# Kernel optimization log

Hardware: AMD Instinct MI355X
Metric: run time of the kernel (lower is better)

The kernel has to match this reference:

```python
import jax, jax.numpy as jnp
import numpy as np

HEADS = 4
DIM_QK = 128
DIM_V = 128
FMAP = 32  # H = W = 32, L = 1024
DIM = 512
B = 16


def rel_to_abs(x):
    # x: [B, Nh, L, 2L-1] -> [B, Nh, L, L]
    b, nh, L, _ = x.shape
    x = jnp.pad(x, ((0, 0), (0, 0), (0, 0), (0, 1)))          # [B, Nh, L, 2L]
    flat = x.reshape(b, nh, L * 2 * L)
    flat = jnp.pad(flat, ((0, 0), (0, 0), (0, L - 1)))
    final = flat.reshape(b, nh, L + 1, 2 * L - 1)
    return final[:, :, :L, L - 1:]


def relative_logits_1d(q, rel_k):
    # q: [B, Nh, H, W, d], rel_k: [2W-1, d] -> [B, Nh, H, H, W, W]
    b, nh, h, w, _ = q.shape
    rl = jnp.einsum('bnhwd,md->bnhwm', q, rel_k)
    rl = rl.reshape(b, nh * h, w, 2 * w - 1)
    rl = rel_to_abs(rl)                                        # [B, Nh*H, W, W]
    rl = rl.reshape(b, nh, h, w, w)
    rl = jnp.broadcast_to(rl[:, :, :, None], (b, nh, h, h, w, w))
    return rl


def rel_pos_logits(q, rel_height, rel_width):
    # q: [B, Nh, L, d] with L = FMAP*FMAP -> [B, Nh, L, L]
    b, nh, L, d = q.shape
    h = w = FMAP
    q5 = q.reshape(b, nh, h, w, d)
    # width logits: 'b n x i y j -> b n (x y) (i j)'
    rw = relative_logits_1d(q5, rel_width)
    rw = rw.transpose(0, 1, 2, 4, 3, 5).reshape(b, nh, h * w, h * w)
    # height logits: transpose spatial, then 'b n x i y j -> b n (y x) (j i)'
    rh = relative_logits_1d(q5.transpose(0, 1, 3, 2, 4), rel_height)
    rh = rh.transpose(0, 1, 4, 2, 5, 3).reshape(b, nh, h * w, h * w)
    return rw + rh


def setup_inputs() -> dict:
    key = jax.random.key(0)
    k1, k2, k3, k4, k5 = jax.random.split(key, 5)
    scale = DIM_QK ** -0.5
    return {
        'featuremap': jax.random.normal(k1, (B, DIM, FMAP, FMAP), jnp.float32),
        'w_qk': jax.random.normal(k2, (2 * HEADS * DIM_QK, DIM), jnp.float32) * (DIM ** -0.5),
        'w_v': jax.random.normal(k3, (HEADS * DIM_V, DIM), jnp.float32) * (DIM ** -0.5),
        'rel_height': jax.random.normal(k4, (2 * FMAP - 1, DIM_QK), jnp.float32) * scale,
        'rel_width': jax.random.normal(k5, (2 * FMAP - 1, DIM_QK), jnp.float32) * scale,
    }


def reference(featuremap, w_qk, w_v, rel_height, rel_width):
    b, c, h, w = featuremap.shape
    L = h * w
    # 1x1 convs (no bias) == channel matmuls
    qk = jnp.einsum('bchw,oc->bohw', featuremap, w_qk)
    q, k = jnp.split(qk, 2, axis=1)
    v = jnp.einsum('bchw,oc->bohw', featuremap, w_v)

    def to_heads(x, d):
        # 'B (h d) H W -> B h (H W) d'
        return x.reshape(b, HEADS, d, L).transpose(0, 1, 3, 2)

    q = to_heads(q, DIM_QK) * (DIM_QK ** -0.5)
    k = to_heads(k, DIM_QK)
    v = to_heads(v, DIM_V)

    logits = jnp.einsum('bhxd,bhyd->bhxy', q, k)
    logits = logits + rel_pos_logits(q, rel_height, rel_width)
    weights = jax.nn.softmax(logits, axis=-1)
    attn = jnp.einsum('bhxy,bhyd->bhxd', weights, v)
    # 'B h (H W) d -> B (h d) H W'
    out = attn.transpose(0, 1, 3, 2).reshape(b, HEADS * DIM_V, h, w)
    return out
```

## Files before the change

### kernel.cpp

```cpp
#include <hip/hip_runtime.h>
#include <hip/hip_bf16.h>
#include <math.h>

typedef __bf16 bf16x8 __attribute__((ext_vector_type(8)));
typedef float f32x4 __attribute__((ext_vector_type(4)));

#define QSCALE_L2E (0.08838834764831845f * 1.4426950408889634f)

static __device__ __forceinline__ unsigned short bits_bf16(float v) {
  __hip_bfloat16 h = __float2bfloat16(v);
  return *reinterpret_cast<unsigned short*>(&h);
}

static __device__ __forceinline__ void gload16(const void* g, void* l) {
  __builtin_amdgcn_global_load_lds(
      (const __attribute__((address_space(1))) void*)g,
      (__attribute__((address_space(3))) void*)l, 16, 0, 0);
}

__global__ __launch_bounds__(256) void k_convw(const float* __restrict__ wqk,
                                               const float* __restrict__ wv,
                                               const float* __restrict__ relw,
                                               const float* __restrict__ relh,
                                               __hip_bfloat16* __restrict__ wall,
                                               __hip_bfloat16* __restrict__ relsb) {
  int i = blockIdx.x * 256 + threadIdx.x;
  if (i < 1536 * 512) {
    float v = (i < 1024 * 512) ? wqk[i] : wv[i - 1024 * 512];
    wall[i] = __float2bfloat16(v);
  } else {
    int j = i - 1536 * 512;
    int t = j >> 13, m = (j >> 7) & 63, d = j & 127;
    float v = (m < 63) ? (t ? relh[m * 128 + d] : relw[m * 128 + d]) : 0.f;
    relsb[j] = __float2bfloat16(v);
  }
}

__global__ __launch_bounds__(256) void k_tfm(const float* __restrict__ fm,
                                             __hip_bfloat16* __restrict__ fmt) {
  __shared__ float t[64][65];
  int lt = blockIdx.x, ct = blockIdx.y, b = blockIdx.z;
  int tid = threadIdx.x;
  const float* src = fm + ((size_t)b * 512 + ct * 64) * 1024 + lt * 64;
#pragma unroll
  for (int i = 0; i < 16; ++i) {
    int idx = i * 256 + tid;
    int r = idx >> 6, cl = idx & 63;
    t[r][cl] = src[(size_t)r * 1024 + cl];
  }
  __syncthreads();
  __hip_bfloat16* dst = fmt + ((size_t)b * 1024 + lt * 64) * 512 + ct * 64;
#pragma unroll
  for (int i = 0; i < 16; ++i) {
    int idx = i * 256 + tid;
    int r = idx >> 6, cc = idx & 63;
    dst[(size_t)r * 512 + cc] = __float2bfloat16(t[cc][r]);
  }
}

__global__ __launch_bounds__(256) void k_gemm(const __hip_bfloat16* __restrict__ fmt,
                                              const __hip_bfloat16* __restrict__ wall,
                                              __hip_bfloat16* __restrict__ Qb,
                                              __hip_bfloat16* __restrict__ Kb,
                                              __hip_bfloat16* __restrict__ Vt) {
  __shared__ char smem[32768];
  char* As = smem;
  char* Bs = smem + 16384;
  int bm = blockIdx.x, bn = blockIdx.y, b = blockIdx.z;
  int tid = threadIdx.x;
  int lane = tid & 63, wave = tid >> 6;
  int wr = wave >> 1, wc = wave & 1;
  int g = lane >> 4, ln = lane & 15;
  const char* Ag = (const char*)(fmt + ((size_t)b * 1024 + bm * 128) * 512);
  const char* Bg = (const char*)(wall + (size_t)bn * 128 * 512);

  int j3 = lane >> 3, j7 = lane & 7;
  int segsrc = ((j7 ^ j3) << 4);

  f32x4 acc[4][4] = {};
  for (int kb = 0; kb < 8; ++kb) {
#pragma unroll
    for (int i = 0; i < 4; ++i) {
      int R = (wave * 4 + i) * 8;
      size_t go = (size_t)(R + j3) * 1024 + (size_t)kb * 128 + segsrc;
      gload16(Ag + go, As + R * 128);
      gload16(Bg + go, Bs + R * 128);
    }
    __syncthreads();
#pragma unroll
    for (int ks = 0; ks < 2; ++ks) {
      int kcol = ks * 64 + (g << 4);
      bf16x8 af[4], bfr[4];
#pragma unroll
      for (int m = 0; m < 4; ++m) {
        int row = wr * 64 + m * 16 + ln;
        af[m] = *(const bf16x8*)(As + row * 128 + (kcol ^ ((ln & 7) << 4)));
      }
#pragma unroll
      for (int n = 0; n < 4; ++n) {
        int row = wc * 64 + n * 16 + ln;
        bfr[n] = *(const bf16x8*)(Bs + row * 128 + (kcol ^ ((ln & 7) << 4)));
      }
#pragma unroll
      for (int m = 0; m < 4; ++m)
#pragma unroll
        for (int n = 0; n < 4; ++n)
          acc[m][n] = __builtin_amdgcn_mfma_f32_16x16x32_bf16(af[m], bfr[n], acc[m][n], 0, 0, 0);
    }
    __syncthreads();
  }

  int otype = bn >> 2;
  int head = bn & 3;
  if (otype != 2) {
    float sc = (otype == 0) ? QSCALE_L2E : 1.0f;
#pragma unroll
    for (int m = 0; m < 4; ++m)
#pragma unroll
      for (int n = 0; n < 4; ++n) {
        int d = wc * 64 + n * 16 + ln;
#pragma unroll
        for (int r = 0; r < 4; ++r) {
          int l = wr * 64 + m * 16 + g * 4 + r;
          *(__hip_bfloat16*)(smem + l * 256 + ((d * 2) ^ ((l & 7) << 4))) =
              __float2bfloat16(acc[m][n][r] * sc);
        }
      }
    __syncthreads();
    __hip_bfloat16* dstb =
        (otype == 0 ? Qb : Kb) + (((size_t)(b * 4 + head) * 1024) + bm * 128) * 128;
#pragma unroll
    for (int i = 0; i < 8; ++i) {
      int idx = i * 256 + tid;
      int row = idx >> 4, c16 = idx & 15;
      uint4 v = *(const uint4*)(smem + row * 256 + ((c16 * 16) ^ ((row & 7) << 4)));
      *(uint4*)(dstb + (size_t)row * 128 + c16 * 8) = v;
    }
  } else {
#pragma unroll
    for (int m = 0; m < 4; ++m)
#pragma unroll
      for (int n = 0; n < 4; ++n) {
        int d = wc * 64 + n * 16 + ln;
        int lbase = wr * 64 + m * 16 + g * 4;
        ushort4 pk;
        pk.x = bits_bf16(acc[m][n][0]);
        pk.y = bits_bf16(acc[m][n][1]);
        pk.z = bits_bf16(acc[m][n][2]);
        pk.w = bits_bf16(acc[m][n][3]);
        *(ushort4*)(smem + d * 256 + ((lbase * 2) ^ ((d & 7) << 4))) = pk;
      }
    __syncthreads();
    __hip_bfloat16* dstb = Vt + ((size_t)(b * 4 + head) * 128) * 1024 + bm * 128;
#pragma unroll
    for (int i = 0; i < 8; ++i) {
      int idx = i * 256 + tid;
      int row = idx >> 4, c16 = idx & 15;
      uint4 v = *(const uint4*)(smem + row * 256 + ((c16 * 16) ^ ((row & 7) << 4)));
      *(uint4*)(dstb + (size_t)row * 1024 + c16 * 8) = v;
    }
  }
}

__global__ __launch_bounds__(256) void k_bias(const __hip_bfloat16* __restrict__ Qb,
                                              const __hip_bfloat16* __restrict__ relsb,
                                              float* __restrict__ QRW,
                                              float* __restrict__ QRH) {
  __shared__ char sh[32768];
  int bx = blockIdx.x, bh = blockIdx.y;
  int tid = threadIdx.x, lane = tid & 63, wave = tid >> 6;
  int g = lane >> 4, ln = lane & 15;
#pragma unroll
  for (int i = 0; i < 8; ++i) {
    int chunk = i * 256 + tid;
    int row = chunk >> 4, c16 = chunk & 15;
    *(uint4*)(sh + row * 256 + ((c16 * 16) ^ ((row & 7) << 4))) =
        *(const uint4*)(relsb + (size_t)row * 128 + c16 * 8);
  }
  __syncthreads();
  size_t bhL = (size_t)bh * 1024;
  int l0 = bx * 128 + wave * 32;
  const __hip_bfloat16* Qg = Qb + (bhL + l0) * 128;
  bf16x8 a[2][4];
#pragma unroll
  for (int lf = 0; lf < 2; ++lf)
#pragma unroll
    for (int ks = 0; ks < 4; ++ks)
      a[lf][ks] = *(const bf16x8*)(Qg + (size_t)(lf * 16 + ln) * 128 + ks * 32 + g * 8);
#pragma unroll
  for (int t = 0; t < 2; ++t) {
    float* dst = (t == 0 ? QRW : QRH) + (bhL + l0) * 64;
#pragma unroll
    for (int n = 0; n < 4; ++n) {
      f32x4 acc2[2] = {};
#pragma unroll
      for (int ks = 0; ks < 4; ++ks) {
        int mrow = n * 16 + ln;
        bf16x8 bf = *(const bf16x8*)(sh + t * 16384 + mrow * 256 +
                                     ((ks * 64 + g * 16) ^ ((mrow & 7) << 4)));
#pragma unroll
        for (int lf = 0; lf < 2; ++lf)
          acc2[lf] = __builtin_amdgcn_mfma_f32_16x16x32_bf16(a[lf][ks], bf, acc2[lf], 0, 0, 0);
      }
#pragma unroll
      for (int lf = 0; lf < 2; ++lf)
#pragma unroll
        for (int r = 0; r < 4; ++r)
          dst[(size_t)(lf * 16 + g * 4 + r) * 64 + n * 16 + ln] = acc2[lf][r];
    }
  }
}

__global__ __launch_bounds__(512, 2) void k_attn(const __hip_bfloat16* __restrict__ Qb,
                                                 const __hip_bfloat16* __restrict__ Kb,
                                                 const __hip_bfloat16* __restrict__ Vt,
                                                 const float* __restrict__ QRW,
                                                 const float* __restrict__ QRH,
                                                 float* __restrict__ out) {
  extern __shared__ char smem[];
  float* hb_s = (float*)smem;
  char* kbuf = smem + 40960;
  char* vbuf = smem + 40960 + 32768;
  char* pt = smem + 40960 + 65536;

  int bh = blockIdx.x, qt = blockIdx.y;
  int b = bh >> 2, h = bh & 3;
  int tid = threadIdx.x, lane = tid & 63, wave = tid >> 6;
  int g = lane >> 4, ln = lane & 15;
  int q0 = qt * 256;
  size_t bhL = (size_t)bh * 1024;

#pragma unroll
  for (int i = 0; i < 5; ++i) {
    int c = i * 512 + tid;
    if (c < 2304) {
      int row = c / 9, j = c % 9;
      int s0 = (31 - ((q0 + row) >> 5)) & ~3;
      *(uint4*)(hb_s + row * 40 + j * 4) =
          *(const uint4*)(QRH + (bhL + q0 + row) * 64 + s0 + j * 4);
    }
  }

  bf16x8 qa[2][4];
  float wb[2][2][4];
  int qloc[2], hbase[2];
#pragma unroll
  for (int u = 0; u < 2; ++u) {
    qloc[u] = wave * 32 + u * 16 + ln;
    int qg = q0 + qloc[u];
    int cx = qg & 31, rx = qg >> 5;
    hbase[u] = (31 - rx) & 3;
    const __hip_bfloat16* qrow = Qb + (bhL + qg) * 128;
#pragma unroll
    for (int ks = 0; ks < 4; ++ks)
      qa[u][ks] = *(const bf16x8*)(qrow + ks * 32 + g * 8);
    const float* wrow = QRW + (bhL + qg) * 64 + (31 - cx) + g * 4;
#pragma unroll
    for (int half = 0; half < 2; ++half)
#pragma unroll
      for (int r = 0; r < 4; ++r) wb[u][half][r] = wrow[half * 16 + r];
  }

  const char* Kg0 = (const char*)(Kb + bhL * 128);
  const char* Vg0 = (const char*)(Vt + (size_t)bh * 128 * 1024);
  int j3 = lane >> 3, j7 = lane & 7;
  int segv = ((j7 ^ j3) << 4);

  auto STAGE = [&](int bsel, int kt2) {
    const char* Kg = Kg0 + (size_t)kt2 * 64 * 256;
    char* kvb = kbuf + bsel * 16384;
#pragma unroll
    for (int i = 0; i < 2; ++i) {
      int R = (wave * 2 + i) * 4;
      int seg = ((lane & 15) ^ ((i & 1) * 4 + (lane >> 4))) << 4;
      gload16(Kg + (size_t)(R + (lane >> 4)) * 256 + seg, kvb + R * 256);
    }
    const char* Vg = Vg0 + (size_t)kt2 * 128;
    char* vtb = vbuf + bsel * 16384;
#pragma unroll
    for (int i = 0; i < 2; ++i) {
      int R = (wave * 2 + i) * 8;
      gload16(Vg + (size_t)(R + j3) * 2048 + segv, vtb + R * 128);
    }
  };

  f32x4 acc[2][8] = {};
  float mrow[2] = {-1e30f, -1e30f}, lrow[2] = {0.f, 0.f};
  char* pw = pt + wave * 4096;

  STAGE(0, 0);
  __syncthreads();

  for (int kt = 0; kt < 16; ++kt) {
    int cur = kt & 1;
    if (kt < 15) STAGE(cur ^ 1, kt + 1);
    char* kvb = kbuf + cur * 16384;
    char* vtb = vbuf + cur * 16384;

    f32x4 s[2][4] = {};
    __builtin_amdgcn_s_setprio(1);
#pragma unroll
    for (int ks = 0; ks < 4; ++ks) {
      int kcol = ks * 64 + (g << 4);
#pragma unroll
      for (int n = 0; n < 4; ++n) {
        int krow = n * 16 + ln;
        bf16x8 kf = *(const bf16x8*)(kvb + krow * 256 + (kcol ^ ((krow & 7) << 4)));
        s[0][n] = __builtin_amdgcn_mfma_f32_16x16x32_bf16(kf, qa[0][ks], s[0][n], 0, 0, 0);
        s[1][n] = __builtin_amdgcn_mfma_f32_16x16x32_bf16(kf, qa[1][ks], s[1][n], 0, 0, 0);
      }
    }
    __builtin_amdgcn_s_setprio(0);
#pragma unroll
    for (int u = 0; u < 2; ++u) {
      float hb0 = hb_s[qloc[u] * 40 + hbase[u] + kt * 2];
      float hb1 = hb_s[qloc[u] * 40 + hbase[u] + kt * 2 + 1];
#pragma unroll
      for (int n = 0; n < 4; ++n) {
        float hb = (n >> 1) ? hb1 : hb0;
#pragma unroll
        for (int r = 0; r < 4; ++r) s[u][n][r] += wb[u][n & 1][r] + hb;
      }
      float mt = s[u][0][0];
#pragma unroll
      for (int n = 0; n < 4; ++n)
#pragma unroll
        for (int r = 0; r < 4; ++r) mt = fmaxf(mt, s[u][n][r]);
      mt = fmaxf(mt, __shfl_xor(mt, 16, 64));
      mt = fmaxf(mt, __shfl_xor(mt, 32, 64));
      float mn = fmaxf(mrow[u], mt);
      float alpha = exp2f(mrow[u] - mn);
      mrow[u] = mn;
      float rs = 0.f;
#pragma unroll
      for (int n = 0; n < 4; ++n)
#pragma unroll
        for (int r = 0; r < 4; ++r) {
          s[u][n][r] = exp2f(s[u][n][r] - mn);
          rs += s[u][n][r];
        }
      rs += __shfl_xor(rs, 16, 64);
      rs += __shfl_xor(rs, 32, 64);
      lrow[u] = lrow[u] * alpha + rs;
#pragma unroll
      for (int mf = 0; mf < 8; ++mf) acc[u][mf] *= alpha;
#pragma unroll
      for (int n = 0; n < 4; ++n) {
        ushort4 pk;
        pk.x = bits_bf16(s[u][n][0]);
        pk.y = bits_bf16(s[u][n][1]);
        pk.z = bits_bf16(s[u][n][2]);
        pk.w = bits_bf16(s[u][n][3]);
        *(ushort4*)(pw + (u * 16 + ln) * 128 + ((n * 32 + g * 8) ^ ((ln & 7) << 4))) = pk;
      }
    }
    __builtin_amdgcn_s_setprio(1);
#pragma unroll
    for (int ks2 = 0; ks2 < 2; ++ks2) {
      int kcb = ks2 * 64 + (g << 4);
      bf16x8 pb0 = *(const bf16x8*)(pw + ln * 128 + (kcb ^ ((ln & 7) << 4)));
      bf16x8 pb1 = *(const bf16x8*)(pw + (16 + ln) * 128 + (kcb ^ ((ln & 7) << 4)));
#pragma unroll
      for (int mf = 0; mf < 8; ++mf) {
        int vrow = mf * 16 + ln;
        bf16x8 av = *(const bf16x8*)(vtb + vrow * 128 + (kcb ^ ((vrow & 7) << 4)));
        acc[0][mf] = __builtin_amdgcn_mfma_f32_16x16x32_bf16(av, pb0, acc[0][mf], 0, 0, 0);
        acc[1][mf] = __builtin_amdgcn_mfma_f32_16x16x32_bf16(av, pb1, acc[1][mf], 0, 0, 0);
      }
    }
    __builtin_amdgcn_s_setprio(0);
    __syncthreads();
  }
#pragma unroll
  for (int u = 0; u < 2; ++u) {
    float linv = 1.0f / lrow[u];
    int qg3 = q0 + wave * 32 + u * 16 + ln;
#pragma unroll
    for (int mf = 0; mf < 8; ++mf) {
      int dbase = mf * 16 + g * 4;
#pragma unroll
      for (int r = 0; r < 4; ++r) {
        out[((size_t)(b * 512 + h * 128 + dbase + r)) * 1024 + qg3] = acc[u][mf][r] * linv;
      }
    }
  }
}

extern "C" void kernel_launch(void* const* d_in, const int* in_sizes, int n_in,
                              void* d_out, int out_size, void* d_ws, size_t ws_size,
                              hipStream_t stream) {
  const float* fm = (const float*)d_in[0];
  const float* wqk = (const float*)d_in[1];
  const float* wv = (const float*)d_in[2];
  const float* relh = (const float*)d_in[3];
  const float* relw = (const float*)d_in[4];
  float* out = (float*)d_out;
  char* w = (char*)d_ws;

  __hip_bfloat16* fmt = (__hip_bfloat16*)w;
  __hip_bfloat16* wall = (__hip_bfloat16*)(w + 16777216);
  __hip_bfloat16* Qb = (__hip_bfloat16*)(w + 18350080);
  __hip_bfloat16* Kb = (__hip_bfloat16*)(w + 35127296);
  __hip_bfloat16* Vt = (__hip_bfloat16*)(w + 51904512);
  float* QRW = (float*)(w + 68681728);
  float* QRH = (float*)(w + 85458944);
  __hip_bfloat16* relsb = (__hip_bfloat16*)(w + 102236160);

  hipFuncSetAttribute((const void*)k_attn,
                      hipFuncAttributeMaxDynamicSharedMemorySize, 139264);

  k_convw<<<3136, 256, 0, stream>>>(wqk, wv, relw, relh, wall, relsb);
  k_tfm<<<dim3(16, 8, 16), 256, 0, stream>>>(fm, fmt);
  k_gemm<<<dim3(8, 12, 16), 256, 0, stream>>>(fmt, wall, Qb, Kb, Vt);
  k_bias<<<dim3(8, 64), 256, 0, stream>>>(Qb, relsb, QRW, QRH);
  k_attn<<<dim3(64, 4), 512, 139264, stream>>>(Qb, Kb, Vt, QRW, QRH, out);
}
```

Before: 125.4 us.

## Shrink attention LDS, skip softmax rescale lazily, raise occupancy bound

Removes the shared-memory staging of height bias and loads it per tile from global memory. It halves the per-wave P buffer, dropping the swizzle, and interleaves P writes with the PV MFMAs. Rescaling of the accumulator is skipped unless the row max grows by more than a threshold. Launch bounds ask for 4 blocks per CU to raise occupancy, which risks register spills given the large accumulator, while the grid only fills about one block per CU.

```diff
diff --git a/kernel.cpp b/kernel.cpp
--- a/kernel.cpp
+++ b/kernel.cpp
@@ -211,17 +211,18 @@
   }
 }
 
-__global__ __launch_bounds__(512, 2) void k_attn(const __hip_bfloat16* __restrict__ Qb,
+__global__ __launch_bounds__(512, 4) void k_attn(const __hip_bfloat16* __restrict__ Qb,
                                                  const __hip_bfloat16* __restrict__ Kb,
                                                  const __hip_bfloat16* __restrict__ Vt,
                                                  const float* __restrict__ QRW,
                                                  const float* __restrict__ QRH,
                                                  float* __restrict__ out) {
   extern __shared__ char smem[];
-  float* hb_s = (float*)smem;
-  char* kbuf = smem + 40960;
-  char* vbuf = smem + 40960 + 32768;
-  char* pt = smem + 40960 + 65536;
+  char* kb0 = smem;
+  char* kb1 = smem + 16384;
+  char* vb0 = smem + 32768;
+  char* vb1 = smem + 49152;
+  char* pt = smem + 65536;
 
   int bh = blockIdx.x, qt = blockIdx.y;
   int b = bh >> 2, h = bh & 3;
@@ -230,26 +231,15 @@
   int q0 = qt * 256;
   size_t bhL = (size_t)bh * 1024;
 
-#pragma unroll
-  for (int i = 0; i < 5; ++i) {
-    int c = i * 512 + tid;
-    if (c < 2304) {
-      int row = c / 9, j = c % 9;
-      int s0 = (31 - ((q0 + row) >> 5)) & ~3;
-      *(uint4*)(hb_s + row * 40 + j * 4) =
-          *(const uint4*)(QRH + (bhL + q0 + row) * 64 + s0 + j * 4);
-    }
-  }
-
   bf16x8 qa[2][4];
   float wb[2][2][4];
-  int qloc[2], hbase[2];
+  const float* hptr[2];
+  int qloc[2];
 #pragma unroll
   for (int u = 0; u < 2; ++u) {
     qloc[u] = wave * 32 + u * 16 + ln;
     int qg = q0 + qloc[u];
     int cx = qg & 31, rx = qg >> 5;
-    hbase[u] = (31 - rx) & 3;
     const __hip_bfloat16* qrow = Qb + (bhL + qg) * 128;
 #pragma unroll
     for (int ks = 0; ks < 4; ++ks)
@@ -259,6 +249,7 @@
     for (int half = 0; half < 2; ++half)
 #pragma unroll
       for (int r = 0; r < 4; ++r) wb[u][half][r] = wrow[half * 16 + r];
+    hptr[u] = QRH + (bhL + qg) * 64 + (31 - rx);
   }
 
   const char* Kg0 = (const char*)(Kb + bhL * 128);
@@ -266,17 +257,17 @@
   int j3 = lane >> 3, j7 = lane & 7;
   int segv = ((j7 ^ j3) << 4);
 
-  auto STAGE = [&](int bsel, int kt2) {
+  auto STAGE_K = [&](char* kvb, int kt2) {
     const char* Kg = Kg0 + (size_t)kt2 * 64 * 256;
-    char* kvb = kbuf + bsel * 16384;
 #pragma unroll
     for (int i = 0; i < 2; ++i) {
       int R = (wave * 2 + i) * 4;
       int seg = ((lane & 15) ^ ((i & 1) * 4 + (lane >> 4))) << 4;
       gload16(Kg + (size_t)(R + (lane >> 4)) * 256 + seg, kvb + R * 256);
     }
+  };
+  auto STAGE_V = [&](char* vtb, int kt2) {
     const char* Vg = Vg0 + (size_t)kt2 * 128;
-    char* vtb = vbuf + bsel * 16384;
 #pragma unroll
     for (int i = 0; i < 2; ++i) {
       int R = (wave * 2 + i) * 8;
@@ -286,16 +277,26 @@
 
   f32x4 acc[2][8] = {};
   float mrow[2] = {-1e30f, -1e30f}, lrow[2] = {0.f, 0.f};
-  char* pw = pt + wave * 4096;
-
-  STAGE(0, 0);
+  char* pw = pt + wave * 2048;
+
+  STAGE_K(kb0, 0);
+  STAGE_V(vb0, 0);
   __syncthreads();
 
+  char *kc = kb0, *kn = kb1, *vc = vb0, *vn = vb1;
+
+#pragma unroll 1
   for (int kt = 0; kt < 16; ++kt) {
-    int cur = kt & 1;
-    if (kt < 15) STAGE(cur ^ 1, kt + 1);
-    char* kvb = kbuf + cur * 16384;
-    char* vtb = vbuf + cur * 16384;
+    if (kt < 15) {
+      STAGE_K(kn, kt + 1);
+      STAGE_V(vn, kt + 1);
+    }
+    float hbv[2][2];
+#pragma unroll
+    for (int u = 0; u < 2; ++u) {
+      hbv[u][0] = hptr[u][kt * 2];
+      hbv[u][1] = hptr[u][kt * 2 + 1];
+    }
 
     f32x4 s[2][4] = {};
     __builtin_amdgcn_s_setprio(1);
@@ -305,72 +306,91 @@
 #pragma unroll
       for (int n = 0; n < 4; ++n) {
         int krow = n * 16 + ln;
-        bf16x8 kf = *(const bf16x8*)(kvb + krow * 256 + (kcol ^ ((krow & 7) << 4)));
+        bf16x8 kf = *(const bf16x8*)(kc + krow * 256 + (kcol ^ ((krow & 7) << 4)));
         s[0][n] = __builtin_amdgcn_mfma_f32_16x16x32_bf16(kf, qa[0][ks], s[0][n], 0, 0, 0);
         s[1][n] = __builtin_amdgcn_mfma_f32_16x16x32_bf16(kf, qa[1][ks], s[1][n], 0, 0, 0);
       }
     }
     __builtin_amdgcn_s_setprio(0);
+
+    float mt[2];
 #pragma unroll
     for (int u = 0; u < 2; ++u) {
-      float hb0 = hb_s[qloc[u] * 40 + hbase[u] + kt * 2];
-      float hb1 = hb_s[qloc[u] * 40 + hbase[u] + kt * 2 + 1];
 #pragma unroll
       for (int n = 0; n < 4; ++n) {
-        float hb = (n >> 1) ? hb1 : hb0;
+        float hb = hbv[u][n >> 1];
 #pragma unroll
         for (int r = 0; r < 4; ++r) s[u][n][r] += wb[u][n & 1][r] + hb;
       }
-      float mt = s[u][0][0];
+      float m = s[u][0][0];
 #pragma unroll
       for (int n = 0; n < 4; ++n)
 #pragma unroll
-        for (int r = 0; r < 4; ++r) mt = fmaxf(mt, s[u][n][r]);
-      mt = fmaxf(mt, __shfl_xor(mt, 16, 64));
-      mt = fmaxf(mt, __shfl_xor(mt, 32, 64));
-      float mn = fmaxf(mrow[u], mt);
-      float alpha = exp2f(mrow[u] - mn);
-      mrow[u] = mn;
+        for (int r = 0; r < 4; ++r) m = fmaxf(m, s[u][n][r]);
+      m = fmaxf(m, __shfl_xor(m, 16, 64));
+      mt[u] = fmaxf(m, __shfl_xor(m, 32, 64));
+    }
+    bool grow = (mt[0] > mrow[0] + 8.f) || (mt[1] > mrow[1] + 8.f);
+    if (__any(grow)) {
+#pragma unroll
+      for (int u = 0; u < 2; ++u) {
+        float mn = fmaxf(mrow[u], mt[u]);
+        float alpha = exp2f(mrow[u] - mn);
+        mrow[u] = mn;
+        lrow[u] *= alpha;
+#pragma unroll
+        for (int mf = 0; mf < 8; ++mf) acc[u][mf] *= alpha;
+      }
+    }
+#pragma unroll
+    for (int u = 0; u < 2; ++u) {
       float rs = 0.f;
 #pragma unroll
       for (int n = 0; n < 4; ++n)
 #pragma unroll
         for (int r = 0; r < 4; ++r) {
-          s[u][n][r] = exp2f(s[u][n][r] - mn);
+          s[u][n][r] = exp2f(s[u][n][r] - mrow[u]);
           rs += s[u][n][r];
         }
       rs += __shfl_xor(rs, 16, 64);
       rs += __shfl_xor(rs, 32, 64);
-      lrow[u] = lrow[u] * alpha + rs;
-#pragma unroll
-      for (int mf = 0; mf < 8; ++mf) acc[u][mf] *= alpha;
-#pragma unroll
-      for (int n = 0; n < 4; ++n) {
-        ushort4 pk;
-        pk.x = bits_bf16(s[u][n][0]);
-        pk.y = bits_bf16(s[u][n][1]);
-        pk.z = bits_bf16(s[u][n][2]);
-        pk.w = bits_bf16(s[u][n][3]);
-        *(ushort4*)(pw + (u * 16 + ln) * 128 + ((n * 32 + g * 8) ^ ((ln & 7) << 4))) = pk;
-      }
-    }
-    __builtin_amdgcn_s_setprio(1);
+      lrow[u] += rs;
+    }
+
 #pragma unroll
     for (int ks2 = 0; ks2 < 2; ++ks2) {
+#pragma unroll
+      for (int u = 0; u < 2; ++u) {
+#pragma unroll
+        for (int nn = 0; nn < 2; ++nn) {
+          int n = ks2 * 2 + nn;
+          ushort4 pk;
+          pk.x = bits_bf16(s[u][n][0]);
+          pk.y = bits_bf16(s[u][n][1]);
+          pk.z = bits_bf16(s[u][n][2]);
+          pk.w = bits_bf16(s[u][n][3]);
+          *(ushort4*)(pw + (u * 16 + ln) * 64 + nn * 32 + g * 8) = pk;
+        }
+      }
       int kcb = ks2 * 64 + (g << 4);
-      bf16x8 pb0 = *(const bf16x8*)(pw + ln * 128 + (kcb ^ ((ln & 7) << 4)));
-      bf16x8 pb1 = *(const bf16x8*)(pw + (16 + ln) * 128 + (kcb ^ ((ln & 7) << 4)));
+      bf16x8 pb0 = *(const bf16x8*)(pw + ln * 64 + g * 16);
+      bf16x8 pb1 = *(const bf16x8*)(pw + (16 + ln) * 64 + g * 16);
+      __builtin_amdgcn_s_setprio(1);
 #pragma unroll
       for (int mf = 0; mf < 8; ++mf) {
         int vrow = mf * 16 + ln;
-        bf16x8 av = *(const bf16x8*)(vtb + vrow * 128 + (kcb ^ ((vrow & 7) << 4)));
+        bf16x8 av = *(const bf16x8*)(vc + vrow * 128 + (kcb ^ ((vrow & 7) << 4)));
         acc[0][mf] = __builtin_amdgcn_mfma_f32_16x16x32_bf16(av, pb0, acc[0][mf], 0, 0, 0);
         acc[1][mf] = __builtin_amdgcn_mfma_f32_16x16x32_bf16(av, pb1, acc[1][mf], 0, 0, 0);
       }
-    }
-    __builtin_amdgcn_s_setprio(0);
+      __builtin_amdgcn_s_setprio(0);
+    }
+
     __syncthreads();
-  }
+    char* t = kc; kc = kn; kn = t;
+    char* t2 = vc; vc = vn; vn = t2;
+  }
+
 #pragma unroll
   for (int u = 0; u < 2; ++u) {
     float linv = 1.0f / lrow[u];
@@ -407,11 +427,11 @@
   __hip_bfloat16* relsb = (__hip_bfloat16*)(w + 102236160);
 
   hipFuncSetAttribute((const void*)k_attn,
-                      hipFuncAttributeMaxDynamicSharedMemorySize, 139264);
+                      hipFuncAttributeMaxDynamicSharedMemorySize, 81920);
 
   k_convw<<<3136, 256, 0, stream>>>(wqk, wv, relw, relh, wall, relsb);
   k_tfm<<<dim3(16, 8, 16), 256, 0, stream>>>(fm, fmt);
   k_gemm<<<dim3(8, 12, 16), 256, 0, stream>>>(fmt, wall, Qb, Kb, Vt);
   k_bias<<<dim3(8, 64), 256, 0, stream>>>(Qb, relsb, QRW, QRH);
-  k_attn<<<dim3(64, 4), 512, 139264, stream>>>(Qb, Kb, Vt, QRW, QRH, out);
-}
+  k_attn<<<dim3(64, 4), 512, 81920, stream>>>(Qb, Kb, Vt, QRW, QRH, out);
+}
```

After: 269.2 us. +114.7%, slower.
